# Optimization experiments

Hardware: AMD Instinct MI355X
Metric: run time of the kernel (lower is better)

The kernel has to match this reference:

```python
import jax, jax.numpy as jnp
import numpy as np

N = 4096
NUM_FEATURES = 1870
HIDDEN = 256
EMBED = 16
ALPHA = 0.2
NEG_BIG = -9e15
EPS = 1e-12


def setup_inputs() -> dict:
    key = jax.random.key(0)
    ks = jax.random.split(key, 9)
    x = jax.random.normal(ks[0], (N, NUM_FEATURES), dtype=jnp.float32)
    # sparse-ish binary adjacency mask (avg degree ~ 41) with self loops
    adj = (jax.random.uniform(ks[1], (N, N)) < 0.01).astype(jnp.float32)
    adj = jnp.maximum(adj, jnp.eye(N, dtype=jnp.float32))
    M = jax.random.uniform(ks[2], (N, N), dtype=jnp.float32)
    s1 = 1.0 / np.sqrt(NUM_FEATURES)
    s2 = 1.0 / np.sqrt(HIDDEN)
    W1 = jax.random.normal(ks[3], (NUM_FEATURES, HIDDEN), dtype=jnp.float32) * s1
    a_self1 = jax.random.normal(ks[4], (HIDDEN, 1), dtype=jnp.float32) * s2
    a_neighs1 = jax.random.normal(ks[5], (HIDDEN, 1), dtype=jnp.float32) * s2
    W2 = jax.random.normal(ks[6], (HIDDEN, EMBED), dtype=jnp.float32) * s2
    a_self2 = jax.random.normal(ks[7], (EMBED, 1), dtype=jnp.float32) / np.sqrt(EMBED)
    a_neighs2 = jax.random.normal(ks[8], (EMBED, 1), dtype=jnp.float32) / np.sqrt(EMBED)
    return {"x": x, "adj": adj, "M": M, "W1": W1, "a_self1": a_self1,
            "a_neighs1": a_neighs1, "W2": W2, "a_self2": a_self2, "a_neighs2": a_neighs2}


def gat_layer(x, adj, M, W, a_self, a_neighs, alpha):
    h = x @ W                                  # [N, out]
    f_self = h @ a_self                        # [N, 1]
    f_neigh = h @ a_neighs                     # [N, 1]
    e = jax.nn.leaky_relu((f_self + f_neigh.T) * M, negative_slope=alpha)  # [N, N]
    e = jnp.where(adj > 0, e, NEG_BIG)
    att = jax.nn.softmax(e, axis=1)            # row-stochastic over neighbors
    return jax.nn.elu(att @ h)                 # [N, out]


def reference(x, adj, M, W1, a_self1, a_neighs1, W2, a_self2, a_neighs2):
    h = gat_layer(x, adj, M, W1, a_self1, a_neighs1, ALPHA)
    h = gat_layer(h, adj, M, W2, a_self2, a_neighs2, ALPHA)
    # F.normalize(h, p=2, dim=1): divide by max(norm, eps)
    norm = jnp.maximum(jnp.linalg.norm(h, axis=1, keepdims=True), EPS)
    z = h / norm                               # [N, EMBED]
    A_pred = jax.nn.sigmoid(z @ z.T)           # [N, N]
    return (A_pred, z)
```

## Files before the change

kernel.cpp:

```cpp
#include <hip/hip_runtime.h>
#include <math.h>

#define NN 4096
#define NFEAT 1870
#define KPAD 1920
#define HID 256
#define EMB 16
#define MAXDEG 128

typedef __attribute__((ext_vector_type(8))) short bf16x8;
typedef __attribute__((ext_vector_type(4))) float f32x4;

__device__ __forceinline__ ushort f2bf(float f) {
    unsigned u = __builtin_bit_cast(unsigned, f);
    u += 0x7fffu + ((u >> 16) & 1u);
    return (ushort)(u >> 16);
}
__device__ __forceinline__ float bf2f(ushort h) {
    unsigned u = ((unsigned)h) << 16;
    return __builtin_bit_cast(float, u);
}

__global__ __launch_bounds__(256) void gemm_xw1(
    const float* __restrict__ Af,
    const ushort* __restrict__ BTh, const ushort* __restrict__ BTl, int ldb,
    int lda, int Kreal, int CHUNK,
    float* __restrict__ Cpart, int Ncols)
{
    __shared__ ushort Ah[128 * 32];
    __shared__ ushort Al[128 * 32];
    __shared__ ushort Bh[64 * 32];
    __shared__ ushort Bl[64 * 32];

    const int tid = threadIdx.x;
    const int lane = tid & 63;
    const int w = tid >> 6;
    const int wr = w >> 1, wc = w & 1;
    const int row0 = blockIdx.x * 128;
    const int col0 = blockIdx.y * 64;
    const int kbeg = blockIdx.z * CHUNK;
    const int kend = min(Kreal, kbeg + CHUNK);
    const int nsteps = (kend - kbeg + 31) >> 5;

    const int ar = tid >> 1;
    const int as2 = (tid & 1) * 2;
    const int br = tid >> 2;
    const int bs = tid & 3;

    const int fr = lane & 15;
    const int fs = lane >> 4;

    f32x4 acc[4][2] = {};

    for (int ks = 0; ks < nsteps; ++ks) {
        const int k0 = kbeg + (ks << 5);
        {
            size_t base = (size_t)(row0 + ar) * lda;
#pragma unroll
            for (int c = 0; c < 2; ++c) {
                int slot = as2 + c;
                int kk = k0 + slot * 8;
                float v[8];
                if (kk + 8 <= Kreal) {
#pragma unroll
                    for (int j = 0; j < 4; ++j) {
                        float2 t2 = *(const float2*)&Af[base + kk + j * 2];
                        v[j * 2] = t2.x; v[j * 2 + 1] = t2.y;
                    }
                } else {
#pragma unroll
                    for (int j = 0; j < 8; ++j)
                        v[j] = (kk + j < Kreal) ? Af[base + kk + j] : 0.f;
                }
                ushort hh[8], ll[8];
#pragma unroll
                for (int j = 0; j < 8; ++j) {
                    hh[j] = f2bf(v[j]);
                    ll[j] = f2bf(v[j] - bf2f(hh[j]));
                }
                int off = ar * 32 + ((slot ^ ((ar >> 1) & 3)) << 3);
                *(int4*)&Ah[off] = *(int4*)hh;
                *(int4*)&Al[off] = *(int4*)ll;
            }
        }
        {
            size_t base = (size_t)(col0 + br) * ldb + k0 + bs * 8;
            int4 vh = *(const int4*)&BTh[base];
            int4 vl = *(const int4*)&BTl[base];
            int off = br * 32 + ((bs ^ ((br >> 1) & 3)) << 3);
            *(int4*)&Bh[off] = vh;
            *(int4*)&Bl[off] = vl;
        }
        __syncthreads();
        bf16x8 afh[4], afl[4], bfh[2], bfl[2];
#pragma unroll
        for (int m = 0; m < 4; ++m) {
            int r = wr * 64 + m * 16 + fr;
            int off = r * 32 + ((fs ^ ((r >> 1) & 3)) << 3);
            afh[m] = *(const bf16x8*)&Ah[off];
            afl[m] = *(const bf16x8*)&Al[off];
        }
#pragma unroll
        for (int n = 0; n < 2; ++n) {
            int r = wc * 32 + n * 16 + fr;
            int off = r * 32 + ((fs ^ ((r >> 1) & 3)) << 3);
            bfh[n] = *(const bf16x8*)&Bh[off];
            bfl[n] = *(const bf16x8*)&Bl[off];
        }
#pragma unroll
        for (int m = 0; m < 4; ++m)
#pragma unroll
            for (int n = 0; n < 2; ++n) {
                acc[m][n] = __builtin_amdgcn_mfma_f32_16x16x32_bf16(afh[m], bfh[n], acc[m][n], 0, 0, 0);
                acc[m][n] = __builtin_amdgcn_mfma_f32_16x16x32_bf16(afh[m], bfl[n], acc[m][n], 0, 0, 0);
                acc[m][n] = __builtin_amdgcn_mfma_f32_16x16x32_bf16(afl[m], bfh[n], acc[m][n], 0, 0, 0);
            }
        __syncthreads();
    }
    float* Cp = Cpart + (size_t)blockIdx.z * NN * Ncols;
#pragma unroll
    for (int m = 0; m < 4; ++m)
#pragma unroll
        for (int n = 0; n < 2; ++n)
#pragma unroll
            for (int r = 0; r < 4; ++r) {
                int row = row0 + wr * 64 + m * 16 + fs * 4 + r;
                int col = col0 + wc * 32 + n * 16 + fr;
                Cp[(size_t)row * Ncols + col] = acc[m][n][r];
            }
}

__global__ __launch_bounds__(256) void conv_w1t_kernel(
    const float* __restrict__ W1, ushort* __restrict__ Wh, ushort* __restrict__ Wl)
{
    __shared__ float t[64][65];
    const int tid = threadIdx.x;
    const int k0 = blockIdx.x * 64, n0 = blockIdx.y * 64;
    const int kk = tid >> 2, c4 = (tid & 3) * 16;
#pragma unroll
    for (int j = 0; j < 4; ++j) {
        int k = k0 + kk;
        float4 v = make_float4(0.f, 0.f, 0.f, 0.f);
        if (k < NFEAT) v = *(const float4*)&W1[(size_t)k * HID + n0 + c4 + j * 4];
        t[kk][c4 + j * 4 + 0] = v.x; t[kk][c4 + j * 4 + 1] = v.y;
        t[kk][c4 + j * 4 + 2] = v.z; t[kk][c4 + j * 4 + 3] = v.w;
    }
    __syncthreads();
    const int on = tid >> 2, ok4 = (tid & 3) * 16;
#pragma unroll
    for (int j = 0; j < 4; ++j) {
        ushort hh[4], ll[4];
#pragma unroll
        for (int i = 0; i < 4; ++i) {
            float v = t[ok4 + j * 4 + i][on];
            hh[i] = f2bf(v); ll[i] = f2bf(v - bf2f(hh[i]));
        }
        size_t o = (size_t)(n0 + on) * KPAD + k0 + ok4 + j * 4;
        *(ushort4*)&Wh[o] = *(ushort4*)hh;
        *(ushort4*)&Wl[o] = *(ushort4*)ll;
    }
}

__global__ __launch_bounds__(256) void reduce_h1_kernel(
    const float* __restrict__ part, float* __restrict__ h1)
{
    const size_t i = ((size_t)blockIdx.x * 256 + threadIdx.x) * 4;
    float4 s = *(const float4*)&part[i];
#pragma unroll
    for (int ch = 1; ch < 4; ++ch) {
        float4 p = *(const float4*)&part[(size_t)ch * NN * HID + i];
        s.x += p.x; s.y += p.y; s.z += p.z; s.w += p.w;
    }
    *(float4*)&h1[i] = s;
}

__global__ __launch_bounds__(256) void extract_kernel(
    const float* __restrict__ adj, const float* __restrict__ Mmat,
    int* __restrict__ nnz, int* __restrict__ gidx, float* __restrict__ Mg)
{
    __shared__ int sidx[4][MAXDEG];
    const int tid = threadIdx.x;
    const int wv = tid >> 6, lane = tid & 63;
    const int row = blockIdx.x * 4 + wv;

    int base = 0;
#pragma unroll 4
    for (int t = 0; t < 16; ++t) {
        int j0 = t * 256 + lane * 4;
        float4 a = *(const float4*)&adj[(size_t)row * NN + j0];
        float av[4] = {a.x, a.y, a.z, a.w};
#pragma unroll
        for (int c = 0; c < 4; ++c) {
            unsigned long long mb = __ballot(av[c] > 0.f);
            if (av[c] > 0.f) {
                int pos = base + (int)__popcll(mb & ((1ull << lane) - 1ull));
                if (pos < MAXDEG) sidx[wv][pos] = j0 + c;
            }
            base += (int)__popcll(mb);
        }
    }
    const int cnt = min(base, MAXDEG);
    if (lane == 0) nnz[row] = cnt;
    for (int s = lane; s < cnt; s += 64) {
        int j = sidx[wv][s];
        gidx[(size_t)row * MAXDEG + s] = j;
        Mg[(size_t)row * MAXDEG + s] = Mmat[(size_t)row * NN + j];
    }
}

__global__ __launch_bounds__(256) void fvec_kernel(
    const float* __restrict__ h, int D,
    const float* __restrict__ a_s, const float* __restrict__ a_n,
    float* __restrict__ fs, float* __restrict__ fn, int nrows)
{
    const int wv = threadIdx.x >> 6;
    const int lane = threadIdx.x & 63;
    const int row = blockIdx.x * 4 + wv;
    if (row >= nrows) return;
    float s = 0.f, n = 0.f;
    for (int d = lane; d < D; d += 64) {
        float v = h[(size_t)row * D + d];
        s += v * a_s[d];
        n += v * a_n[d];
    }
#pragma unroll
    for (int off = 32; off > 0; off >>= 1) {
        s += __shfl_down(s, off, 64);
        n += __shfl_down(n, off, 64);
    }
    if (lane == 0) { fs[row] = s; fn[row] = n; }
}

__global__ __launch_bounds__(256) void spmm1_kernel(
    const int* __restrict__ nnz, const int* __restrict__ gidx,
    const float* __restrict__ Mg,
    const float* __restrict__ fs, const float* __restrict__ fn,
    const float* __restrict__ h1, float* __restrict__ g1)
{
    __shared__ float p_s[MAXDEG];
    __shared__ int j_s[MAXDEG];
    __shared__ float wred[4], wsum[4];
    const int row = blockIdx.x;
    const int tid = threadIdx.x;
    const int lane = tid & 63, wv = tid >> 6;
    const int cnt = nnz[row];
    const float fsi = fs[row];

    float lmax = -3.0e38f;
    for (int s = tid; s < cnt; s += 256) {
        int j = gidx[(size_t)row * MAXDEG + s];
        j_s[s] = j;
        float e = (fsi + fn[j]) * Mg[(size_t)row * MAXDEG + s];
        e = (e > 0.f) ? e : 0.2f * e;
        p_s[s] = e;
        lmax = fmaxf(lmax, e);
    }
#pragma unroll
    for (int off = 32; off > 0; off >>= 1)
        lmax = fmaxf(lmax, __shfl_down(lmax, off, 64));
    if (lane == 0) wred[wv] = lmax;
    __syncthreads();
    const float m = fmaxf(fmaxf(wred[0], wred[1]), fmaxf(wred[2], wred[3]));

    float lsum = 0.f;
    for (int s = tid; s < cnt; s += 256) {
        float p = expf(p_s[s] - m);
        p_s[s] = p;
        lsum += p;
    }
#pragma unroll
    for (int off = 32; off > 0; off >>= 1)
        lsum += __shfl_down(lsum, off, 64);
    if (lane == 0) wsum[wv] = lsum;
    __syncthreads();
    const float inv = 1.f / (wsum[0] + wsum[1] + wsum[2] + wsum[3]);

    float acc = 0.f;
#pragma unroll 4
    for (int s = 0; s < cnt; ++s)
        acc += p_s[s] * h1[(size_t)j_s[s] * HID + tid];
    float v = acc * inv;
    v = (v > 0.f) ? v : expm1f(v);
    g1[(size_t)row * HID + tid] = v;
}

__global__ __launch_bounds__(256) void spmm2_kernel(
    const int* __restrict__ nnz, const int* __restrict__ gidx,
    const float* __restrict__ Mg,
    const float* __restrict__ fs, const float* __restrict__ fn,
    const float* __restrict__ h2, float* __restrict__ z)
{
    __shared__ float p_s[4][MAXDEG];
    __shared__ int j_s[4][MAXDEG];
    const int tid = threadIdx.x;
    const int wv = tid >> 6, lane = tid & 63;
    const int row = blockIdx.x * 4 + wv;
    const int cnt = nnz[row];
    const float fsi = fs[row];

    float lmax = -3.0e38f;
    for (int s = lane; s < cnt; s += 64) {
        int j = gidx[(size_t)row * MAXDEG + s];
        j_s[wv][s] = j;
        float e = (fsi + fn[j]) * Mg[(size_t)row * MAXDEG + s];
        e = (e > 0.f) ? e : 0.2f * e;
        p_s[wv][s] = e;
        lmax = fmaxf(lmax, e);
    }
#pragma unroll
    for (int off = 1; off < 64; off <<= 1)
        lmax = fmaxf(lmax, __shfl_xor(lmax, off, 64));

    float lsum = 0.f;
    for (int s = lane; s < cnt; s += 64) {
        float p = expf(p_s[wv][s] - lmax);
        p_s[wv][s] = p;
        lsum += p;
    }
#pragma unroll
    for (int off = 1; off < 64; off <<= 1)
        lsum += __shfl_xor(lsum, off, 64);
    const float inv = 1.f / lsum;

    const int s0 = lane >> 4, d = lane & 15;
    float acc = 0.f;
    for (int s = s0; s < cnt; s += 4)
        acc += p_s[wv][s] * h2[(size_t)j_s[wv][s] * EMB + d];
    acc += __shfl_xor(acc, 16, 64);
    acc += __shfl_xor(acc, 32, 64);

    float v = acc * inv;
    v = (v > 0.f) ? v : expm1f(v);
    float ss = v * v;
#pragma unroll
    for (int off = 1; off < 16; off <<= 1)
        ss += __shfl_xor(ss, off, 64);
    float zn = v / fmaxf(sqrtf(ss), 1e-12f);
    if (lane < 16) z[(size_t)row * EMB + lane] = zn;
}

__global__ __launch_bounds__(256) void gemm_h2_kernel(
    const float* __restrict__ g1, const float* __restrict__ W2,
    float* __restrict__ h2)
{
    __shared__ float Ws[256][16];
    __shared__ float Gs[16][257];
    const int tid = threadIdx.x;
    const int row0 = blockIdx.x * 16;
#pragma unroll
    for (int i = 0; i < 16; ++i) {
        int idx = tid + i * 256;
        Ws[idx >> 4][idx & 15] = W2[idx];
    }
#pragma unroll
    for (int i = 0; i < 16; ++i) {
        int idx = tid + i * 256;
        Gs[idx >> 8][idx & 255] = g1[(size_t)(row0 + (idx >> 8)) * HID + (idx & 255)];
    }
    __syncthreads();
    const int r = tid >> 4, c = tid & 15;
    float acc = 0.f;
#pragma unroll 8
    for (int k = 0; k < 256; ++k)
        acc += Gs[r][k] * Ws[k][c];
    h2[(size_t)(row0 + r) * EMB + c] = acc;
}

__global__ __launch_bounds__(256) void apred_kernel(
    const float* __restrict__ z, float* __restrict__ out)
{
    __shared__ float zr[64][20];
    __shared__ float zc[64][20];
    const int tid = threadIdx.x;
    const int r0 = blockIdx.y * 64, c0 = blockIdx.x * 64;
#pragma unroll
    for (int i = 0; i < 4; ++i) {
        int idx = tid + i * 256;
        int rr = idx >> 4, d = idx & 15;
        zr[rr][d] = z[(size_t)(r0 + rr) * EMB + d];
        zc[rr][d] = z[(size_t)(c0 + rr) * EMB + d];
    }
    __syncthreads();
    const int tx = tid & 15, ty = tid >> 4;
    float rb[4][16], cb[4][16];
#pragma unroll
    for (int i = 0; i < 4; ++i)
#pragma unroll
        for (int d = 0; d < 16; ++d) {
            rb[i][d] = zr[ty * 4 + i][d];
            cb[i][d] = zc[tx * 4 + i][d];
        }
#pragma unroll
    for (int i = 0; i < 4; ++i) {
        float4 o;
        float v[4];
#pragma unroll
        for (int j = 0; j < 4; ++j) {
            float s = 0.f;
#pragma unroll
            for (int d = 0; d < 16; ++d) s += rb[i][d] * cb[j][d];
            v[j] = 1.f / (1.f + expf(-s));
        }
        o.x = v[0]; o.y = v[1]; o.z = v[2]; o.w = v[3];
        *reinterpret_cast<float4*>(
            &out[(size_t)(r0 + ty * 4 + i) * NN + c0 + tx * 4]) = o;
    }
}

extern "C" void kernel_launch(void* const* d_in, const int* in_sizes, int n_in,
                              void* d_out, int out_size, void* d_ws, size_t ws_size,
                              hipStream_t stream)
{
    const float* x    = (const float*)d_in[0];
    const float* adj  = (const float*)d_in[1];
    const float* Mm   = (const float*)d_in[2];
    const float* W1   = (const float*)d_in[3];
    const float* a_s1 = (const float*)d_in[4];
    const float* a_n1 = (const float*)d_in[5];
    const float* W2   = (const float*)d_in[6];
    const float* a_s2 = (const float*)d_in[7];
    const float* a_n2 = (const float*)d_in[8];

    float* out = (float*)d_out;
    float* z   = out + (size_t)NN * NN;

    char* w = (char*)d_ws;
    float* part  = (float*)w;  w += (size_t)4 * NN * HID * 4;
    float* h1    = (float*)w;  w += (size_t)NN * HID * 4;
    float* g1    = (float*)w;  w += (size_t)NN * HID * 4;
    ushort* W1Th = (ushort*)w; w += (size_t)HID * KPAD * 2;
    ushort* W1Tl = (ushort*)w; w += (size_t)HID * KPAD * 2;
    float* h2    = (float*)w;  w += (size_t)NN * EMB * 4;
    int*   nnzp  = (int*)w;    w += NN * 4;
    int*   gidx  = (int*)w;    w += (size_t)NN * MAXDEG * 4;
    float* Mg    = (float*)w;  w += (size_t)NN * MAXDEG * 4;
    float* fs1   = (float*)w;  w += NN * 4;
    float* fn1   = (float*)w;  w += NN * 4;
    float* fs2   = (float*)w;  w += NN * 4;
    float* fn2   = (float*)w;  w += NN * 4;

    extract_kernel<<<NN / 4, 256, 0, stream>>>(adj, Mm, nnzp, gidx, Mg);

    conv_w1t_kernel<<<dim3(30, 4), 256, 0, stream>>>(W1, W1Th, W1Tl);
    gemm_xw1<<<dim3(32, 4, 4), 256, 0, stream>>>(
        x, W1Th, W1Tl, KPAD, NFEAT, NFEAT, 480, part, HID);
    reduce_h1_kernel<<<NN * HID / 1024, 256, 0, stream>>>(part, h1);
    fvec_kernel<<<1024, 256, 0, stream>>>(h1, HID, a_s1, a_n1, fs1, fn1, NN);
    spmm1_kernel<<<NN, 256, 0, stream>>>(nnzp, gidx, Mg, fs1, fn1, h1, g1);

    gemm_h2_kernel<<<256, 256, 0, stream>>>(g1, W2, h2);
    fvec_kernel<<<1024, 256, 0, stream>>>(h2, EMB, a_s2, a_n2, fs2, fn2, NN);
    spmm2_kernel<<<NN / 4, 256, 0, stream>>>(nnzp, gidx, Mg, fs2, fn2, h2, z);

    apred_kernel<<<dim3(64, 64), 256, 0, stream>>>(z, out);
}
```

Baseline: 114.0 us.

## Switch X·W1 to single fp16 MFMA, fuse f-vectors into reductions, use fast exp

Replaces the 3-pass bf16 split-precision GEMM with a single fp16 MFMA pass over pre-converted x and W1. The new GEMM uses 64-wide K steps with register prefetch of the next tile. The attention f-vector dot products are fused into the h1 partial-sum reduction and the h2 GEMM, removing two fvec launches. expf and expm1f are replaced by __expf throughout. This cuts MFMA work and launches, but fp16 rounding of x and W1 lowers accuracy and adds an extra pass that writes x out as fp16.

```diff
diff --git a/kernel.cpp b/kernel.cpp
--- a/kernel.cpp
+++ b/kernel.cpp
@@ -8,130 +8,40 @@
 #define EMB 16
 #define MAXDEG 128
 
-typedef __attribute__((ext_vector_type(8))) short bf16x8;
+typedef __attribute__((ext_vector_type(8))) _Float16 f16x8;
 typedef __attribute__((ext_vector_type(4))) float f32x4;
 
-__device__ __forceinline__ ushort f2bf(float f) {
-    unsigned u = __builtin_bit_cast(unsigned, f);
-    u += 0x7fffu + ((u >> 16) & 1u);
-    return (ushort)(u >> 16);
-}
-__device__ __forceinline__ float bf2f(ushort h) {
-    unsigned u = ((unsigned)h) << 16;
-    return __builtin_bit_cast(float, u);
-}
-
-__global__ __launch_bounds__(256) void gemm_xw1(
-    const float* __restrict__ Af,
-    const ushort* __restrict__ BTh, const ushort* __restrict__ BTl, int ldb,
-    int lda, int Kreal, int CHUNK,
-    float* __restrict__ Cpart, int Ncols)
-{
-    __shared__ ushort Ah[128 * 32];
-    __shared__ ushort Al[128 * 32];
-    __shared__ ushort Bh[64 * 32];
-    __shared__ ushort Bl[64 * 32];
-
-    const int tid = threadIdx.x;
-    const int lane = tid & 63;
-    const int w = tid >> 6;
-    const int wr = w >> 1, wc = w & 1;
-    const int row0 = blockIdx.x * 128;
-    const int col0 = blockIdx.y * 64;
-    const int kbeg = blockIdx.z * CHUNK;
-    const int kend = min(Kreal, kbeg + CHUNK);
-    const int nsteps = (kend - kbeg + 31) >> 5;
-
-    const int ar = tid >> 1;
-    const int as2 = (tid & 1) * 2;
-    const int br = tid >> 2;
-    const int bs = tid & 3;
-
-    const int fr = lane & 15;
-    const int fs = lane >> 4;
-
-    f32x4 acc[4][2] = {};
-
-    for (int ks = 0; ks < nsteps; ++ks) {
-        const int k0 = kbeg + (ks << 5);
-        {
-            size_t base = (size_t)(row0 + ar) * lda;
-#pragma unroll
-            for (int c = 0; c < 2; ++c) {
-                int slot = as2 + c;
-                int kk = k0 + slot * 8;
-                float v[8];
-                if (kk + 8 <= Kreal) {
-#pragma unroll
-                    for (int j = 0; j < 4; ++j) {
-                        float2 t2 = *(const float2*)&Af[base + kk + j * 2];
-                        v[j * 2] = t2.x; v[j * 2 + 1] = t2.y;
-                    }
-                } else {
-#pragma unroll
-                    for (int j = 0; j < 8; ++j)
-                        v[j] = (kk + j < Kreal) ? Af[base + kk + j] : 0.f;
-                }
-                ushort hh[8], ll[8];
-#pragma unroll
-                for (int j = 0; j < 8; ++j) {
-                    hh[j] = f2bf(v[j]);
-                    ll[j] = f2bf(v[j] - bf2f(hh[j]));
-                }
-                int off = ar * 32 + ((slot ^ ((ar >> 1) & 3)) << 3);
-                *(int4*)&Ah[off] = *(int4*)hh;
-                *(int4*)&Al[off] = *(int4*)ll;
-            }
-        }
-        {
-            size_t base = (size_t)(col0 + br) * ldb + k0 + bs * 8;
-            int4 vh = *(const int4*)&BTh[base];
-            int4 vl = *(const int4*)&BTl[base];
-            int off = br * 32 + ((bs ^ ((br >> 1) & 3)) << 3);
-            *(int4*)&Bh[off] = vh;
-            *(int4*)&Bl[off] = vl;
-        }
-        __syncthreads();
-        bf16x8 afh[4], afl[4], bfh[2], bfl[2];
-#pragma unroll
-        for (int m = 0; m < 4; ++m) {
-            int r = wr * 64 + m * 16 + fr;
-            int off = r * 32 + ((fs ^ ((r >> 1) & 3)) << 3);
-            afh[m] = *(const bf16x8*)&Ah[off];
-            afl[m] = *(const bf16x8*)&Al[off];
-        }
-#pragma unroll
-        for (int n = 0; n < 2; ++n) {
-            int r = wc * 32 + n * 16 + fr;
-            int off = r * 32 + ((fs ^ ((r >> 1) & 3)) << 3);
-            bfh[n] = *(const bf16x8*)&Bh[off];
-            bfl[n] = *(const bf16x8*)&Bl[off];
-        }
-#pragma unroll
-        for (int m = 0; m < 4; ++m)
-#pragma unroll
-            for (int n = 0; n < 2; ++n) {
-                acc[m][n] = __builtin_amdgcn_mfma_f32_16x16x32_bf16(afh[m], bfh[n], acc[m][n], 0, 0, 0);
-                acc[m][n] = __builtin_amdgcn_mfma_f32_16x16x32_bf16(afh[m], bfl[n], acc[m][n], 0, 0, 0);
-                acc[m][n] = __builtin_amdgcn_mfma_f32_16x16x32_bf16(afl[m], bfh[n], acc[m][n], 0, 0, 0);
-            }
-        __syncthreads();
-    }
-    float* Cp = Cpart + (size_t)blockIdx.z * NN * Ncols;
-#pragma unroll
-    for (int m = 0; m < 4; ++m)
-#pragma unroll
-        for (int n = 0; n < 2; ++n)
-#pragma unroll
-            for (int r = 0; r < 4; ++r) {
-                int row = row0 + wr * 64 + m * 16 + fs * 4 + r;
-                int col = col0 + wc * 32 + n * 16 + fr;
-                Cp[(size_t)row * Ncols + col] = acc[m][n][r];
-            }
+__device__ __forceinline__ ushort f2h(float f) {
+    _Float16 h = (_Float16)f;
+    return __builtin_bit_cast(ushort, h);
+}
+
+__global__ __launch_bounds__(256) void xcv_kernel(
+    const float* __restrict__ x, ushort* __restrict__ xf)
+{
+    const int idx = blockIdx.x * 256 + threadIdx.x;
+    const int row = idx / 240;
+    const int c0 = (idx % 240) * 8;
+    float v[8];
+    if (c0 + 8 <= NFEAT) {
+#pragma unroll
+        for (int j = 0; j < 4; ++j) {
+            float2 t = *(const float2*)&x[(size_t)row * NFEAT + c0 + j * 2];
+            v[j * 2] = t.x; v[j * 2 + 1] = t.y;
+        }
+    } else {
+#pragma unroll
+        for (int j = 0; j < 8; ++j)
+            v[j] = (c0 + j < NFEAT) ? x[(size_t)row * NFEAT + c0 + j] : 0.f;
+    }
+    ushort u[8];
+#pragma unroll
+    for (int j = 0; j < 8; ++j) u[j] = f2h(v[j]);
+    *(int4*)&xf[(size_t)row * KPAD + c0] = *(int4*)u;
 }
 
 __global__ __launch_bounds__(256) void conv_w1t_kernel(
-    const float* __restrict__ W1, ushort* __restrict__ Wh, ushort* __restrict__ Wl)
+    const float* __restrict__ W1, ushort* __restrict__ Wh)
 {
     __shared__ float t[64][65];
     const int tid = threadIdx.x;
@@ -149,29 +59,134 @@
     const int on = tid >> 2, ok4 = (tid & 3) * 16;
 #pragma unroll
     for (int j = 0; j < 4; ++j) {
-        ushort hh[4], ll[4];
-#pragma unroll
-        for (int i = 0; i < 4; ++i) {
-            float v = t[ok4 + j * 4 + i][on];
-            hh[i] = f2bf(v); ll[i] = f2bf(v - bf2f(hh[i]));
-        }
+        ushort hh[4];
+#pragma unroll
+        for (int i = 0; i < 4; ++i)
+            hh[i] = f2h(t[ok4 + j * 4 + i][on]);
         size_t o = (size_t)(n0 + on) * KPAD + k0 + ok4 + j * 4;
         *(ushort4*)&Wh[o] = *(ushort4*)hh;
-        *(ushort4*)&Wl[o] = *(ushort4*)ll;
-    }
-}
-
-__global__ __launch_bounds__(256) void reduce_h1_kernel(
-    const float* __restrict__ part, float* __restrict__ h1)
-{
-    const size_t i = ((size_t)blockIdx.x * 256 + threadIdx.x) * 4;
-    float4 s = *(const float4*)&part[i];
+    }
+}
+
+__global__ __launch_bounds__(256) void gemm_xw1(
+    const ushort* __restrict__ Ag,
+    const ushort* __restrict__ Bg,
+    float* __restrict__ Cpart)
+{
+    __shared__ ushort Ah[128 * 64];
+    __shared__ ushort Bh[64 * 64];
+    const int tid = threadIdx.x;
+    const int lane = tid & 63;
+    const int w = tid >> 6;
+    const int wr = w >> 1, wc = w & 1;
+    const int row0 = blockIdx.x * 128;
+    const int col0 = blockIdx.y * 64;
+    const int kbeg = blockIdx.z * 512;
+    const int kend = min(KPAD, kbeg + 512);
+    const int nsteps = (kend - kbeg) >> 6;
+
+    const int fr = lane & 15, fs = lane >> 4;
+
+    const int a_row = tid >> 1;
+    const int a_sk0 = (tid & 1) * 4;
+    const int b_row = tid >> 2;
+    const int b_sk0 = (tid & 3) * 2;
+
+    const size_t a_gbase = (size_t)(row0 + a_row) * KPAD;
+    const size_t b_gbase = (size_t)(col0 + b_row) * KPAD;
+
+    int4 ra[4], rb[2];
+#define LOADAB(K0)                                                        \
+    {                                                                     \
+        _Pragma("unroll")                                                 \
+        for (int i = 0; i < 4; ++i)                                       \
+            ra[i] = *(const int4*)&Ag[a_gbase + (K0) + (a_sk0 + i) * 8];  \
+        _Pragma("unroll")                                                 \
+        for (int i = 0; i < 2; ++i)                                       \
+            rb[i] = *(const int4*)&Bg[b_gbase + (K0) + (b_sk0 + i) * 8];  \
+    }
+
+    LOADAB(kbeg);
+    f32x4 acc[4][2] = {};
+
+    for (int ks = 0; ks < nsteps; ++ks) {
+        __syncthreads();
+#pragma unroll
+        for (int i = 0; i < 4; ++i)
+            *(int4*)&Ah[(a_row * 8 + ((a_sk0 + i) ^ (a_row & 7))) * 8] = ra[i];
+#pragma unroll
+        for (int i = 0; i < 2; ++i)
+            *(int4*)&Bh[(b_row * 8 + ((b_sk0 + i) ^ (b_row & 7))) * 8] = rb[i];
+        __syncthreads();
+        if (ks + 1 < nsteps) LOADAB(kbeg + (ks + 1) * 64);
+
+        f16x8 af[4][2], bf[2][2];
+#pragma unroll
+        for (int m = 0; m < 4; ++m) {
+            int r = wr * 64 + m * 16 + fr;
+#pragma unroll
+            for (int kf = 0; kf < 2; ++kf) {
+                int sk = kf * 4 + fs;
+                af[m][kf] = *(const f16x8*)&Ah[(r * 8 + (sk ^ (r & 7))) * 8];
+            }
+        }
+#pragma unroll
+        for (int n = 0; n < 2; ++n) {
+            int r = wc * 32 + n * 16 + fr;
+#pragma unroll
+            for (int kf = 0; kf < 2; ++kf) {
+                int sk = kf * 4 + fs;
+                bf[n][kf] = *(const f16x8*)&Bh[(r * 8 + (sk ^ (r & 7))) * 8];
+            }
+        }
+#pragma unroll
+        for (int m = 0; m < 4; ++m)
+#pragma unroll
+            for (int n = 0; n < 2; ++n)
+#pragma unroll
+                for (int kf = 0; kf < 2; ++kf)
+                    acc[m][n] = __builtin_amdgcn_mfma_f32_16x16x32_f16(
+                        af[m][kf], bf[n][kf], acc[m][n], 0, 0, 0);
+    }
+    float* Cp = Cpart + (size_t)blockIdx.z * NN * HID;
+#pragma unroll
+    for (int m = 0; m < 4; ++m)
+#pragma unroll
+        for (int n = 0; n < 2; ++n)
+#pragma unroll
+            for (int r = 0; r < 4; ++r) {
+                int row = row0 + wr * 64 + m * 16 + fs * 4 + r;
+                int col = col0 + wc * 32 + n * 16 + fr;
+                Cp[(size_t)row * HID + col] = acc[m][n][r];
+            }
+}
+
+__global__ __launch_bounds__(256) void reduce_h1f_kernel(
+    const float* __restrict__ part, float* __restrict__ h1,
+    const float* __restrict__ a_s, const float* __restrict__ a_n,
+    float* __restrict__ fs, float* __restrict__ fn)
+{
+    const int tid = threadIdx.x, wv = tid >> 6, lane = tid & 63;
+    const int row = blockIdx.x * 4 + wv;
+    const int d0 = lane * 4;
+    const size_t o = (size_t)row * HID + d0;
+    float4 s = *(const float4*)&part[o];
 #pragma unroll
     for (int ch = 1; ch < 4; ++ch) {
-        float4 p = *(const float4*)&part[(size_t)ch * NN * HID + i];
+        float4 p = *(const float4*)&part[(size_t)ch * NN * HID + o];
         s.x += p.x; s.y += p.y; s.z += p.z; s.w += p.w;
     }
-    *(float4*)&h1[i] = s;
+    *(float4*)&h1[o] = s;
+    float4 as4 = *(const float4*)&a_s[d0];
+    float4 an4 = *(const float4*)&a_n[d0];
+    float ps = s.x * as4.x + s.y * as4.y + s.z * as4.z + s.w * as4.w;
+    float pn = s.x * an4.x + s.y * an4.y + s.z * an4.z + s.w * an4.w;
+#pragma unroll
+    for (int off = 32; off > 0; off >>= 1) {
+        ps += __shfl_down(ps, off, 64);
+        pn += __shfl_down(pn, off, 64);
+    }
+    if (lane == 0) { fs[row] = ps; fn[row] = pn; }
 }
 
 __global__ __launch_bounds__(256) void extract_kernel(
@@ -206,29 +221,6 @@
         gidx[(size_t)row * MAXDEG + s] = j;
         Mg[(size_t)row * MAXDEG + s] = Mmat[(size_t)row * NN + j];
     }
-}
-
-__global__ __launch_bounds__(256) void fvec_kernel(
-    const float* __restrict__ h, int D,
-    const float* __restrict__ a_s, const float* __restrict__ a_n,
-    float* __restrict__ fs, float* __restrict__ fn, int nrows)
-{
-    const int wv = threadIdx.x >> 6;
-    const int lane = threadIdx.x & 63;
-    const int row = blockIdx.x * 4 + wv;
-    if (row >= nrows) return;
-    float s = 0.f, n = 0.f;
-    for (int d = lane; d < D; d += 64) {
-        float v = h[(size_t)row * D + d];
-        s += v * a_s[d];
-        n += v * a_n[d];
-    }
-#pragma unroll
-    for (int off = 32; off > 0; off >>= 1) {
-        s += __shfl_down(s, off, 64);
-        n += __shfl_down(n, off, 64);
-    }
-    if (lane == 0) { fs[row] = s; fn[row] = n; }
 }
 
 __global__ __launch_bounds__(256) void spmm1_kernel(
@@ -264,7 +256,7 @@
 
     float lsum = 0.f;
     for (int s = tid; s < cnt; s += 256) {
-        float p = expf(p_s[s] - m);
+        float p = __expf(p_s[s] - m);
         p_s[s] = p;
         lsum += p;
     }
@@ -280,8 +272,45 @@
     for (int s = 0; s < cnt; ++s)
         acc += p_s[s] * h1[(size_t)j_s[s] * HID + tid];
     float v = acc * inv;
-    v = (v > 0.f) ? v : expm1f(v);
+    v = (v > 0.f) ? v : (__expf(v) - 1.f);
     g1[(size_t)row * HID + tid] = v;
+}
+
+__global__ __launch_bounds__(256) void gemm_h2_kernel(
+    const float* __restrict__ g1, const float* __restrict__ W2,
+    const float* __restrict__ a_s2, const float* __restrict__ a_n2,
+    float* __restrict__ h2, float* __restrict__ fs2, float* __restrict__ fn2)
+{
+    __shared__ float Ws[256][16];
+    __shared__ float Gs[16][257];
+    const int tid = threadIdx.x;
+    const int row0 = blockIdx.x * 16;
+#pragma unroll
+    for (int i = 0; i < 16; ++i) {
+        int idx = tid + i * 256;
+        Ws[idx >> 4][idx & 15] = W2[idx];
+    }
+#pragma unroll
+    for (int i = 0; i < 16; ++i) {
+        int idx = tid + i * 256;
+        Gs[idx >> 8][idx & 255] = g1[(size_t)(row0 + (idx >> 8)) * HID + (idx & 255)];
+    }
+    __syncthreads();
+    const int r = tid >> 4, c = tid & 15;
+    float acc = 0.f;
+#pragma unroll 8
+    for (int k = 0; k < 256; ++k)
+        acc += Gs[r][k] * Ws[k][c];
+    h2[(size_t)(row0 + r) * EMB + c] = acc;
+
+    float ps = acc * a_s2[c];
+    float pn = acc * a_n2[c];
+#pragma unroll
+    for (int off = 1; off < 16; off <<= 1) {
+        ps += __shfl_xor(ps, off, 64);
+        pn += __shfl_xor(pn, off, 64);
+    }
+    if (c == 0) { fs2[row0 + r] = ps; fn2[row0 + r] = pn; }
 }
 
 __global__ __launch_bounds__(256) void spmm2_kernel(
@@ -313,7 +342,7 @@
 
     float lsum = 0.f;
     for (int s = lane; s < cnt; s += 64) {
-        float p = expf(p_s[wv][s] - lmax);
+        float p = __expf(p_s[wv][s] - lmax);
         p_s[wv][s] = p;
         lsum += p;
     }
@@ -330,40 +359,13 @@
     acc += __shfl_xor(acc, 32, 64);
 
     float v = acc * inv;
-    v = (v > 0.f) ? v : expm1f(v);
+    v = (v > 0.f) ? v : (__expf(v) - 1.f);
     float ss = v * v;
 #pragma unroll
     for (int off = 1; off < 16; off <<= 1)
         ss += __shfl_xor(ss, off, 64);
     float zn = v / fmaxf(sqrtf(ss), 1e-12f);
     if (lane < 16) z[(size_t)row * EMB + lane] = zn;
-}
-
-__global__ __launch_bounds__(256) void gemm_h2_kernel(
-    const float* __restrict__ g1, const float* __restrict__ W2,
-    float* __restrict__ h2)
-{
-    __shared__ float Ws[256][16];
-    __shared__ float Gs[16][257];
-    const int tid = threadIdx.x;
-    const int row0 = blockIdx.x * 16;
-#pragma unroll
-    for (int i = 0; i < 16; ++i) {
-        int idx = tid + i * 256;
-        Ws[idx >> 4][idx & 15] = W2[idx];
-    }
-#pragma unroll
-    for (int i = 0; i < 16; ++i) {
-        int idx = tid + i * 256;
-        Gs[idx >> 8][idx & 255] = g1[(size_t)(row0 + (idx >> 8)) * HID + (idx & 255)];
-    }
-    __syncthreads();
-    const int r = tid >> 4, c = tid & 15;
-    float acc = 0.f;
-#pragma unroll 8
-    for (int k = 0; k < 256; ++k)
-        acc += Gs[r][k] * Ws[k][c];
-    h2[(size_t)(row0 + r) * EMB + c] = acc;
 }
 
 __global__ __launch_bounds__(256) void apred_kernel(
@@ -399,7 +401,7 @@
             float s = 0.f;
 #pragma unroll
             for (int d = 0; d < 16; ++d) s += rb[i][d] * cb[j][d];
-            v[j] = 1.f / (1.f + expf(-s));
+            v[j] = 1.f / (1.f + __expf(-s));
         }
         o.x = v[0]; o.y = v[1]; o.z = v[2]; o.w = v[3];
         *reinterpret_cast<float4*>(
@@ -428,8 +430,8 @@
     float* part  = (float*)w;  w += (size_t)4 * NN * HID * 4;
     float* h1    = (float*)w;  w += (size_t)NN * HID * 4;
     float* g1    = (float*)w;  w += (size_t)NN * HID * 4;
+    ushort* xf16 = (ushort*)w; w += (size_t)NN * KPAD * 2;
     ushort* W1Th = (ushort*)w; w += (size_t)HID * KPAD * 2;
-    ushort* W1Tl = (ushort*)w; w += (size_t)HID * KPAD * 2;
     float* h2    = (float*)w;  w += (size_t)NN * EMB * 4;
     int*   nnzp  = (int*)w;    w += NN * 4;
     int*   gidx  = (int*)w;    w += (size_t)NN * MAXDEG * 4;
@@ -439,17 +441,15 @@
     float* fs2   = (float*)w;  w += NN * 4;
     float* fn2   = (float*)w;  w += NN * 4;
 
+    xcv_kernel<<<NN * 240 / 256, 256, 0, stream>>>(x, xf16);
+    conv_w1t_kernel<<<dim3(30, 4), 256, 0, stream>>>(W1, W1Th);
     extract_kernel<<<NN / 4, 256, 0, stream>>>(adj, Mm, nnzp, gidx, Mg);
 
-    conv_w1t_kernel<<<dim3(30, 4), 256, 0, stream>>>(W1, W1Th, W1Tl);
-    gemm_xw1<<<dim3(32, 4, 4), 256, 0, stream>>>(
-        x, W1Th, W1Tl, KPAD, NFEAT, NFEAT, 480, part, HID);
-    reduce_h1_kernel<<<NN * HID / 1024, 256, 0, stream>>>(part, h1);
-    fvec_kernel<<<1024, 256, 0, stream>>>(h1, HID, a_s1, a_n1, fs1, fn1, NN);
+    gemm_xw1<<<dim3(32, 4, 4), 256, 0, stream>>>(xf16, W1Th, part);
+    reduce_h1f_kernel<<<NN / 4, 256, 0, stream>>>(part, h1, a_s1, a_n1, fs1, fn1);
     spmm1_kernel<<<NN, 256, 0, stream>>>(nnzp, gidx, Mg, fs1, fn1, h1, g1);
 
-    gemm_h2_kernel<<<256, 256, 0, stream>>>(g1, W2, h2);
-    fvec_kernel<<<1024, 256, 0, stream>>>(h2, EMB, a_s2, a_n2, fs2, fn2, NN);
+    gemm_h2_kernel<<<256, 256, 0, stream>>>(g1, W2, a_s2, a_n2, h2, fs2, fn2);
     spmm2_kernel<<<NN / 4, 256, 0, stream>>>(nnzp, gidx, Mg, fs2, fn2, h2, z);
 
     apred_kernel<<<dim3(64, 64), 256, 0, stream>>>(z, out);
```

After: 117.7 us. +3.2%, slower.
